# Kernel tuning notes

Hardware: AMD Instinct MI355X
Metric: run time of the kernel (lower is better)

Reference implementation:

```python
import jax, jax.numpy as jnp
import numpy as np

EMBED = 1024
N_HEADS = 16
HEAD_DIM = EMBED // N_HEADS
B, T = 2, 2048


def setup_inputs() -> dict:
    key = jax.random.key(0)
    k1, k2, k3 = jax.random.split(key, 3)
    x = jax.random.normal(k1, (B, T, EMBED), dtype=jnp.float32)
    # torch nn.Linear(embed, 3*embed, bias=False): weight [3C, C]; store as [C, 3C] for x @ W
    w_attn = jax.random.normal(k2, (EMBED, 3 * EMBED), dtype=jnp.float32) * (EMBED ** -0.5)
    w_proj = jax.random.normal(k3, (EMBED, EMBED), dtype=jnp.float32) * (EMBED ** -0.5)
    return {"x": x, "w_attn": w_attn, "w_proj": w_proj}


def reference(x, w_attn, w_proj):
    Bb, Tt, C = x.shape
    kqv = x @ w_attn  # [B, T, 3C]
    # NOTE: original code unpacks as k, q, v (k first)
    k, q, v = jnp.split(kqv, 3, axis=2)
    def heads(t):
        return t.reshape(Bb, Tt, N_HEADS, HEAD_DIM).transpose(0, 2, 1, 3)  # [B, H, T, D]
    k, q, v = heads(k), heads(q), heads(v)
    scale = HEAD_DIM ** -0.5
    wei = jnp.einsum("bhqd,bhkd->bhqk", q, k) * scale  # [B, H, T, T]
    mask = jnp.tril(jnp.ones((Tt, Tt), dtype=bool))
    wei = jnp.where(mask[None, None], wei, -jnp.inf)
    wei = jax.nn.softmax(wei, axis=-1)
    y = jnp.einsum("bhqk,bhkd->bhqd", wei, v)  # [B, H, T, D]
    y = y.transpose(0, 2, 1, 3).reshape(Bb, Tt, C)
    return y @ w_proj
```

## Files before the change

kernel.cpp:

```cpp
#include <hip/hip_runtime.h>

typedef unsigned short u16;
typedef unsigned int u32;

typedef __attribute__((ext_vector_type(4))) float f32x4;
typedef __attribute__((ext_vector_type(8))) short s16x8;

__device__ __forceinline__ u16 f2bf(float f) {
    u32 u = __builtin_bit_cast(u32, f);
    u += 0x7fffu + ((u >> 16) & 1u);
    return (u16)(u >> 16);
}

__device__ __forceinline__ u32 pk_bf16(float a, float b) {
    return (u32)f2bf(a) | ((u32)f2bf(b) << 16);
}

__device__ __forceinline__ u32 cvtpk(float a, float b) {
    u32 r;
    asm("v_cvt_pk_bf16_f32 %0, %1, %2" : "=v"(r) : "v"(a), "v"(b));
    return r;
}

__device__ __forceinline__ float bf2f(u16 h) {
    u32 u = ((u32)h) << 16;
    return __builtin_bit_cast(float, u);
}

#define EXP2(x) exp2f(x)

__device__ __forceinline__ void gload16(const u16* g, u16* l) {
    __builtin_amdgcn_global_load_lds(
        (const __attribute__((address_space(1))) void*)(const void*)g,
        (__attribute__((address_space(3))) void*)(void*)l, 16, 0, 0);
}

__global__ void k_cast(const float* __restrict__ in, u16* __restrict__ out) {
    int i = (blockIdx.x * 256 + threadIdx.x) * 4;
    float4 v = *(const float4*)(in + i);
    uint2 pk;
    pk.x = pk_bf16(v.x, v.y);
    pk.y = pk_bf16(v.z, v.w);
    *(uint2*)(out + i) = pk;
}

__global__ void k_transpose(const float* __restrict__ in, u16* __restrict__ out,
                            int K, int N) {
    __shared__ float tile[32][33];
    int n0 = blockIdx.x * 32, k0 = blockIdx.y * 32;
    int x = threadIdx.x, y = threadIdx.y;
#pragma unroll
    for (int j = 0; j < 32; j += 8)
        tile[y + j][x] = in[(size_t)(k0 + y + j) * N + n0 + x];
    __syncthreads();
#pragma unroll
    for (int j = 0; j < 32; j += 8)
        out[(size_t)(n0 + y + j) * K + k0 + x] = f2bf(tile[x][y + j]);
}

template <int EPI>
__global__ __launch_bounds__(256, 2) void k_gemm(
        const u16* __restrict__ A, const u16* __restrict__ Bt,
        void* __restrict__ Cout, u16* __restrict__ Vt, int N, int K) {
    __shared__ u16 As[128 * 32];
    __shared__ u16 Bs[128 * 32];
    const int nbn = N >> 7;
    const int bm = (int)blockIdx.x / nbn, bn = (int)blockIdx.x % nbn;
    const int tid = threadIdx.x;
    const int wv = tid >> 6, ln = tid & 63;
    const int lg = ln >> 4, lr = ln & 15;
    const int wr = (wv >> 1) << 6, wc = (wv & 1) << 6;

    const u16* gA = A + (size_t)(bm * 128 + wv * 32 + (ln >> 2)) * K + (ln & 3) * 8;
    const u16* gB = Bt + (size_t)(bn * 128 + wv * 32 + (ln >> 2)) * K + (ln & 3) * 8;
    u16* lA = As + wv * 1024;
    u16* lB = Bs + wv * 1024;

    f32x4 acc[4][4] = {};

    for (int k0 = 0; k0 < K; k0 += 32) {
        gload16(gA + k0, lA);
        gload16(gA + k0 + 16 * K, lA + 512);
        gload16(gB + k0, lB);
        gload16(gB + k0 + 16 * K, lB + 512);
        __syncthreads();
        s16x8 af[4], bf[4];
#pragma unroll
        for (int mi = 0; mi < 4; ++mi)
            af[mi] = *(const s16x8*)&As[(wr + mi * 16 + lr) * 32 + lg * 8];
#pragma unroll
        for (int ni = 0; ni < 4; ++ni)
            bf[ni] = *(const s16x8*)&Bs[(wc + ni * 16 + lr) * 32 + lg * 8];
#pragma unroll
        for (int mi = 0; mi < 4; ++mi)
#pragma unroll
            for (int ni = 0; ni < 4; ++ni)
                acc[mi][ni] = __builtin_amdgcn_mfma_f32_16x16x32_bf16(
                        af[mi], bf[ni], acc[mi][ni], 0, 0, 0);
        __syncthreads();
    }

    const int crow0 = bm * 128 + wr + lg * 4;
    const int ccol0 = bn * 128 + wc + lr;
    if (EPI == 0) {
        float* Co = (float*)Cout;
#pragma unroll
        for (int mi = 0; mi < 4; ++mi)
#pragma unroll
            for (int ni = 0; ni < 4; ++ni)
#pragma unroll
                for (int r = 0; r < 4; ++r)
                    Co[(size_t)(crow0 + mi * 16 + r) * N + ccol0 + ni * 16] =
                            acc[mi][ni][r];
    } else {
        if (bn < 16) {
            const float qs = (bn >= 8) ? 0.18033688011112042f : 1.0f;
            u16* Co = (u16*)Cout;
#pragma unroll
            for (int mi = 0; mi < 4; ++mi)
#pragma unroll
                for (int ni = 0; ni < 4; ++ni)
#pragma unroll
                    for (int r = 0; r < 4; ++r)
                        Co[(size_t)(crow0 + mi * 16 + r) * 3072 + ccol0 + ni * 16] =
                                f2bf(acc[mi][ni][r] * qs);
        } else {
#pragma unroll
            for (int mi = 0; mi < 4; ++mi) {
                int row = crow0 + mi * 16;
                int bb = row >> 11, t = row & 2047;
#pragma unroll
                for (int ni = 0; ni < 4; ++ni) {
                    int hd = ccol0 + ni * 16 - 2048;
                    uint2 pk;
                    pk.x = pk_bf16(acc[mi][ni][0], acc[mi][ni][1]);
                    pk.y = pk_bf16(acc[mi][ni][2], acc[mi][ni][3]);
                    *(uint2*)&Vt[(size_t)(bb * 1024 + hd) * 2048 + t] = pk;
                }
            }
        }
    }
}

__global__ __launch_bounds__(512, 4) void k_attn(
        const u16* __restrict__ kqv, const u16* __restrict__ Vt,
        u16* __restrict__ y) {
    const int orig = blockIdx.x;
    const int xcd = orig & 7, slot = orig >> 3;
    const int bh = xcd * 4 + (slot >> 4);
    const int pr = slot & 15;
    const int b = bh >> 4, h = bh & 15;
    const int tid = threadIdx.x;
    const int wave = tid >> 6;
    const int g = wave >> 2;
    const int wv4 = wave & 3;
    const int lane = tid & 63;
    const int lg = lane >> 4, lr = lane & 15;

    __shared__ u16 Ks[2][2][64 * 64];
    __shared__ u16 Vs[2][2][64 * 64];
    __shared__ u16 Ps[8][16 * 64];
    u16* comb = &Ps[0][0];

    const u16* Kg = kqv + (size_t)b * 2048 * 3072 + h * 64;
    const u16* Qg = Kg + 1024;
    const u16* Vg = Vt + (size_t)bh * 64 * 2048;

    const int srow = wv4 * 16 + (lane >> 3);
    const int cK = (lane & 7) ^ (lane >> 3);
    const u16* kg0 = Kg + (size_t)srow * 3072 + cK * 8;
    const u16* vg0 = Vg + (size_t)srow * 2048 + cK * 8;
    const int swz = lr & 7;

    s16x8 ones;
#pragma unroll
    for (int i = 0; i < 8; ++i) ones[i] = (short)0x3F80;

    u16* Psw = &Ps[wave][0];

#define STAGE(bb, t)                                      \
    {                                                     \
        const u16* kp_ = kg0 + (size_t)(t) * 64 * 3072;   \
        const u16* vp_ = vg0 + (size_t)(t) * 64;          \
        u16* lk_ = &Ks[g][bb][wv4 * 1024];                \
        u16* lv_ = &Vs[g][bb][wv4 * 1024];                \
        gload16(kp_, lk_);                                \
        gload16(kp_ + 8 * 3072, lk_ + 512);               \
        gload16(vp_, lv_);                                \
        gload16(vp_ + 8 * 2048, lv_ + 512);               \
    }

    for (int pass = 0; pass < 2; ++pass) {
        const int qt = pass ? (31 - pr) : pr;
        const int nkt = qt + 1;
        const int iters = (nkt + 1) >> 1;
        const int qbase = qt * 64 + wv4 * 16;

        const u16* qrp = Qg + (size_t)(qbase + lr) * 3072;
        const s16x8 qf0 = *(const s16x8*)(qrp + lg * 8);
        const s16x8 qf1 = *(const s16x8*)(qrp + 32 + lg * 8);

        f32x4 o[4] = {};
        f32x4 l4 = {};

        if (g < nkt) STAGE(0, g);
        asm volatile("s_waitcnt vmcnt(0)\n\ts_barrier" ::: "memory");

        for (int i = 0; i < iters; ++i) {
            const int cur = i & 1;
            const int t = 2 * i + g;
            if (t + 2 < nkt) STAGE(cur ^ 1, t + 2);
            if (t < nkt) {
                f32x4 st[4];
                __builtin_amdgcn_s_setprio(1);
#pragma unroll
                for (int kb = 0; kb < 4; ++kb) {
                    const int row = kb * 16 + lr;
                    s16x8 kf0 = *(const s16x8*)&Ks[g][cur][row * 64 + ((lg ^ swz) << 3)];
                    s16x8 kf1 = *(const s16x8*)&Ks[g][cur][row * 64 + (((4 + lg) ^ swz) << 3)];
                    f32x4 z = {};
                    z = __builtin_amdgcn_mfma_f32_16x16x32_bf16(kf0, qf0, z, 0, 0, 0);
                    z = __builtin_amdgcn_mfma_f32_16x16x32_bf16(kf1, qf1, z, 0, 0, 0);
                    st[kb] = z;
                }
                __builtin_amdgcn_s_setprio(0);

                if (t == nkt - 1) {
                    const int q_abs = qbase + lr;
                    const int kb0 = t * 64 + lg * 4;
#pragma unroll
                    for (int kb = 0; kb < 4; ++kb)
#pragma unroll
                        for (int r = 0; r < 4; ++r)
                            st[kb][r] = EXP2((kb0 + kb * 16 + r <= q_abs)
                                                 ? st[kb][r] : -3e38f);
                } else {
#pragma unroll
                    for (int kb = 0; kb < 4; ++kb)
#pragma unroll
                        for (int r = 0; r < 4; ++r) st[kb][r] = EXP2(st[kb][r]);
                }

#pragma unroll
                for (int kb = 0; kb < 4; ++kb) {
                    const int kbs = (kb + lr) & 3;
                    uint2 w;
                    w.x = cvtpk(st[kb][0], st[kb][1]);
                    w.y = cvtpk(st[kb][2], st[kb][3]);
                    *(uint2*)&Psw[lr * 64 + kbs * 16 + lg * 4] = w;
                }
                asm volatile("s_waitcnt lgkmcnt(0)" ::: "memory");
                __builtin_amdgcn_sched_barrier(0);

                __builtin_amdgcn_s_setprio(1);
#pragma unroll
                for (int half = 0; half < 2; ++half) {
                    const int kbs = ((half * 2 + (lg >> 1)) + lr) & 3;
                    s16x8 pf = *(const s16x8*)&Psw[lr * 64 + kbs * 16 + (lg & 1) * 8];
                    l4 = __builtin_amdgcn_mfma_f32_16x16x32_bf16(ones, pf, l4, 0, 0, 0);
#pragma unroll
                    for (int dt = 0; dt < 4; ++dt) {
                        const int vrow = dt * 16 + lr;
                        s16x8 vf = *(const s16x8*)&Vs[g][cur][vrow * 64 +
                                                    (((half * 4 + lg) ^ swz) << 3)];
                        o[dt] = __builtin_amdgcn_mfma_f32_16x16x32_bf16(vf, pf, o[dt], 0, 0, 0);
                    }
                }
                __builtin_amdgcn_s_setprio(0);
            }
            asm volatile("s_waitcnt vmcnt(0)\n\ts_barrier" ::: "memory");
        }

        __syncthreads();
        if (g == 1) {
            u16* ce = comb + (size_t)(wv4 * 64 + lane) * 20;
#pragma unroll
            for (int dt = 0; dt < 4; ++dt) {
                uint2 w;
                w.x = cvtpk(o[dt][0], o[dt][1]);
                w.y = cvtpk(o[dt][2], o[dt][3]);
                *(uint2*)(ce + dt * 4) = w;
            }
            *(float*)(ce + 16) = l4[0];
        }
        __syncthreads();
        if (g == 0) {
            const u16* ce = comb + (size_t)(wv4 * 64 + lane) * 20;
            float l = l4[0] + *(const float*)(ce + 16);
#pragma unroll
            for (int dt = 0; dt < 4; ++dt) {
                uint2 w = *(const uint2*)(ce + dt * 4);
                o[dt][0] += bf2f((u16)(w.x & 0xffff));
                o[dt][1] += bf2f((u16)(w.x >> 16));
                o[dt][2] += bf2f((u16)(w.y & 0xffff));
                o[dt][3] += bf2f((u16)(w.y >> 16));
            }
            const float inv = 1.0f / l;
            u16* yb = y + (size_t)(b * 2048 + qbase + lr) * 1024 + h * 64;
#pragma unroll
            for (int dt = 0; dt < 4; ++dt) {
                uint2 w;
                w.x = cvtpk(o[dt][0] * inv, o[dt][1] * inv);
                w.y = cvtpk(o[dt][2] * inv, o[dt][3] * inv);
                *(uint2*)(yb + dt * 16 + lg * 4) = w;
            }
        }
        __syncthreads();
    }
#undef STAGE
}

extern "C" void kernel_launch(void* const* d_in, const int* in_sizes, int n_in,
                              void* d_out, int out_size, void* d_ws, size_t ws_size,
                              hipStream_t stream) {
    const float* x = (const float*)d_in[0];
    const float* w_attn = (const float*)d_in[1];
    const float* w_proj = (const float*)d_in[2];
    float* out = (float*)d_out;
    char* ws = (char*)d_ws;

    u16* x_bf = (u16*)(ws);
    u16* wat  = (u16*)(ws + (size_t)(8 << 20));
    u16* wpt  = (u16*)(ws + (size_t)(14 << 20));
    u16* kqv  = (u16*)(ws + (size_t)(16 << 20));
    u16* vt   = (u16*)(ws + (size_t)(40 << 20));
    u16* yb   = (u16*)(ws + (size_t)(48 << 20));

    k_cast<<<4096, 256, 0, stream>>>(x, x_bf);
    k_transpose<<<dim3(96, 32), dim3(32, 8), 0, stream>>>(w_attn, wat, 1024, 3072);
    k_transpose<<<dim3(32, 32), dim3(32, 8), 0, stream>>>(w_proj, wpt, 1024, 1024);
    k_gemm<1><<<32 * 24, 256, 0, stream>>>(x_bf, wat, kqv, vt, 3072, 1024);
    k_attn<<<512, 512, 0, stream>>>(kqv, vt, yb);
    k_gemm<0><<<32 * 8, 256, 0, stream>>>(yb, wpt, out, nullptr, 1024, 1024);
}
```

Measured before the change: 179.2 us.

## Reshuffle softmax probabilities in registers via permlane swaps instead of LDS

The attention kernel previously wrote exponentiated scores to a per-wave LDS buffer and read them back in MFMA B-operand layout. It now packs them to bf16 and uses v_permlane32_swap/v_permlane16_swap to move the values into the needed lane layout directly in registers. This removes the LDS round trip and its wait, and shrinks the shared buffer to just the combine area, which may improve occupancy. The GEMM also gets an XCD-aware block-index swizzle, and one __syncthreads before the combine is dropped, which relies on the preceding barrier and the smaller dedicated buffer being safe.

```diff
diff --git a/kernel.cpp b/kernel.cpp
--- a/kernel.cpp
+++ b/kernel.cpp
@@ -5,6 +5,7 @@
 
 typedef __attribute__((ext_vector_type(4))) float f32x4;
 typedef __attribute__((ext_vector_type(8))) short s16x8;
+typedef __attribute__((ext_vector_type(4))) u32 u32x4;
 
 __device__ __forceinline__ u16 f2bf(float f) {
     u32 u = __builtin_bit_cast(u32, f);
@@ -25,6 +26,13 @@
 __device__ __forceinline__ float bf2f(u16 h) {
     u32 u = ((u32)h) << 16;
     return __builtin_bit_cast(float, u);
+}
+
+__device__ __forceinline__ void pl32swap(u32& a, u32& b) {
+    asm volatile("v_permlane32_swap_b32 %0, %1" : "+v"(a), "+v"(b));
+}
+__device__ __forceinline__ void pl16swap(u32& a, u32& b) {
+    asm volatile("v_permlane16_swap_b32 %0, %1" : "+v"(a), "+v"(b));
 }
 
 #define EXP2(x) exp2f(x)
@@ -65,7 +73,10 @@
     __shared__ u16 As[128 * 32];
     __shared__ u16 Bs[128 * 32];
     const int nbn = N >> 7;
-    const int bm = (int)blockIdx.x / nbn, bn = (int)blockIdx.x % nbn;
+    const int cpx = (int)gridDim.x >> 3;
+    const int bid = (int)blockIdx.x;
+    const int swb = (bid & 7) * cpx + (bid >> 3);
+    const int bm = swb / nbn, bn = swb % nbn;
     const int tid = threadIdx.x;
     const int wv = tid >> 6, ln = tid & 63;
     const int lg = ln >> 4, lr = ln & 15;
@@ -159,8 +170,7 @@
 
     __shared__ u16 Ks[2][2][64 * 64];
     __shared__ u16 Vs[2][2][64 * 64];
-    __shared__ u16 Ps[8][16 * 64];
-    u16* comb = &Ps[0][0];
+    __shared__ u16 comb[4 * 64 * 20];
 
     const u16* Kg = kqv + (size_t)b * 2048 * 3072 + h * 64;
     const u16* Qg = Kg + 1024;
@@ -175,8 +185,6 @@
     s16x8 ones;
 #pragma unroll
     for (int i = 0; i < 8; ++i) ones[i] = (short)0x3F80;
-
-    u16* Psw = &Ps[wave][0];
 
 #define STAGE(bb, t)                                      \
     {                                                     \
@@ -241,22 +249,31 @@
                         for (int r = 0; r < 4; ++r) st[kb][r] = EXP2(st[kb][r]);
                 }
 
-#pragma unroll
-                for (int kb = 0; kb < 4; ++kb) {
-                    const int kbs = (kb + lr) & 3;
-                    uint2 w;
-                    w.x = cvtpk(st[kb][0], st[kb][1]);
-                    w.y = cvtpk(st[kb][2], st[kb][3]);
-                    *(uint2*)&Psw[lr * 64 + kbs * 16 + lg * 4] = w;
-                }
-                asm volatile("s_waitcnt lgkmcnt(0)" ::: "memory");
-                __builtin_amdgcn_sched_barrier(0);
+                u32 E[2][2], O[2][2];
+#pragma unroll
+                for (int kbh = 0; kbh < 2; ++kbh)
+#pragma unroll
+                    for (int hh = 0; hh < 2; ++hh) {
+                        E[kbh][hh] = cvtpk(st[2 * kbh][2 * hh], st[2 * kbh][2 * hh + 1]);
+                        O[kbh][hh] = cvtpk(st[2 * kbh + 1][2 * hh], st[2 * kbh + 1][2 * hh + 1]);
+                    }
+#pragma unroll
+                for (int kbh = 0; kbh < 2; ++kbh)
+#pragma unroll
+                    for (int hh = 0; hh < 2; ++hh) {
+                        pl32swap(E[kbh][hh], O[kbh][hh]);
+                        pl16swap(E[kbh][hh], O[kbh][hh]);
+                    }
 
                 __builtin_amdgcn_s_setprio(1);
 #pragma unroll
                 for (int half = 0; half < 2; ++half) {
-                    const int kbs = ((half * 2 + (lg >> 1)) + lr) & 3;
-                    s16x8 pf = *(const s16x8*)&Psw[lr * 64 + kbs * 16 + (lg & 1) * 8];
+                    u32x4 pw;
+                    pw.x = E[half][0];
+                    pw.y = E[half][1];
+                    pw.z = O[half][0];
+                    pw.w = O[half][1];
+                    s16x8 pf = __builtin_bit_cast(s16x8, pw);
                     l4 = __builtin_amdgcn_mfma_f32_16x16x32_bf16(ones, pf, l4, 0, 0, 0);
 #pragma unroll
                     for (int dt = 0; dt < 4; ++dt) {
@@ -271,7 +288,6 @@
             asm volatile("s_waitcnt vmcnt(0)\n\ts_barrier" ::: "memory");
         }
 
-        __syncthreads();
         if (g == 1) {
             u16* ce = comb + (size_t)(wv4 * 64 + lane) * 20;
 #pragma unroll
```

Result: faster. 172.0 us (-4.0%).
